# Optimization experiments

Measured on AMD Instinct MI355X. Metric: run time of the kernel, lower is better.

Reference implementation:

```python
import jax, jax.numpy as jnp
import numpy as np

N, R, B, OUT, STD = 512, 4, 65536, 512, 0.01


def setup_inputs() -> dict:
    key = jax.random.key(0)
    ks = jax.random.split(key, 6)
    return {
        "x": jax.random.normal(ks[0], (B, N), jnp.float32),
        "G": jax.random.normal(ks[1], (N, R), jnp.float32) * STD,
        "H": jax.random.normal(ks[2], (N, R), jnp.float32) * STD,
        "b1": jax.random.normal(ks[3], (N,), jnp.float32) * STD,
        "W2": jax.random.normal(ks[4], (N, OUT), jnp.float32) * STD,
        "b2": jax.random.normal(ks[5], (OUT,), jnp.float32) * STD,
    }


def _shift_A(v):
    # Z_1 v: circular shift down with corner +1 (Toeplitz-like operator A)
    return jnp.concatenate([v[-1:], v[:-1]], axis=0)


def _shift_BT(v):
    # Z_{-1}^T v: shift up with corner -1 (Toeplitz-like operator B^T)
    return jnp.concatenate([v[1:], -v[:1]], axis=0)


def _krylov(shift_fn, V):
    # K[j, :, i] = A^j v_i, shape (n, n, r)
    def step(v, _):
        return shift_fn(v), v
    _, K = jax.lax.scan(step, V, None, length=V.shape[0])
    return K


def krylov_recon(G, H):
    # W = sum_i Krylov(Z_1, g_i) @ Krylov(Z_{-1}^T, h_i)^T, shape (n, n)
    KA = _krylov(_shift_A, G)   # (n, n, r)
    KB = _krylov(_shift_BT, H)  # (n, n, r)
    return jnp.einsum('jai,jbi->ab', KA, KB)


def reference(x, G, H, b1, W2, b2):
    W = krylov_recon(G, H)                 # (n, n) structured matrix
    h = jax.nn.relu(x @ W + b1)            # (B, n)
    return h @ W2 + b2                     # (B, out)
```

## Files before the change

### kernel.cpp

```cpp
#include <hip/hip_runtime.h>
#include <hip/hip_bf16.h>
#include <stdint.h>


typedef __attribute__((ext_vector_type(8))) short bf16x8;
typedef __attribute__((ext_vector_type(4))) float f32x4;
typedef __attribute__((ext_vector_type(4))) unsigned int u32x4;

__device__ __forceinline__ unsigned short f2bf(float f) {
  return __builtin_bit_cast(unsigned short, __float2bfloat16(f));
}

__global__ void build_w_partials(const float* __restrict__ G, const float* __restrict__ H,
                                 float* __restrict__ Wp) {
  __shared__ float4 Gs[512];
  __shared__ float4 Hs[512];
  const int t = threadIdx.x;
  const float4* G4 = (const float4*)G;
  const float4* H4 = (const float4*)H;
  for (int i = t; i < 512; i += 256) { Gs[i] = G4[i]; Hs[i] = H4[i]; }
  __syncthreads();

  const int blk  = blockIdx.x;
  const int tile = blk >> 2;
  const int jc   = blk & 3;
  const int a0 = (tile >> 3) << 6;
  const int b0 = (tile & 7) << 6;
  const int ab = a0 + ((t >> 4) << 2);
  const int bb = b0 + ((t & 15) << 2);

  float acc[4][4] = {};
  const int j0 = jc << 7;
  for (int jj = 0; jj < 128; ++jj) {
    const int j = j0 + jj;
    float4 Ga[4], Hb[4];
#pragma unroll
    for (int r = 0; r < 4; ++r) Ga[r] = Gs[(ab + r - j) & 511];
#pragma unroll
    for (int c = 0; c < 4; ++c) {
      const int idx = bb + c + j;
      const float s = (idx >= 512) ? -1.f : 1.f;
      const float4 hv = Hs[idx & 511];
      Hb[c].x = hv.x * s; Hb[c].y = hv.y * s; Hb[c].z = hv.z * s; Hb[c].w = hv.w * s;
    }
#pragma unroll
    for (int r = 0; r < 4; ++r)
#pragma unroll
      for (int c = 0; c < 4; ++c)
        acc[r][c] += Ga[r].x * Hb[c].x + Ga[r].y * Hb[c].y +
                     Ga[r].z * Hb[c].z + Ga[r].w * Hb[c].w;
  }

  float* outp = Wp + (size_t)jc * 262144;
#pragma unroll
  for (int r = 0; r < 4; ++r)
#pragma unroll
    for (int c = 0; c < 4; ++c)
      outp[(size_t)(ab + r) * 512 + (bb + c)] = acc[r][c];
}

__global__ void reduce_transpose_w(const float* __restrict__ Wp, unsigned short* __restrict__ Wt) {
  const int idx = blockIdx.x * 256 + threadIdx.x;
  const int b = idx >> 9, a = idx & 511;
  const size_t o = (size_t)a * 512 + b;
  float s = Wp[o] + Wp[o + 262144] + Wp[o + 524288] + Wp[o + 786432];
  Wt[(size_t)b * 512 + a] = f2bf(s);
}

__global__ void transpose_convert_w2(const float* __restrict__ W2, unsigned short* __restrict__ W2t) {
  const int idx = blockIdx.x * 256 + threadIdx.x;
  const int n = idx >> 9, k = idx & 511;
  W2t[(size_t)n * 512 + k] = f2bf(W2[(size_t)k * 512 + n]);
}

template <bool AF32>
__global__ __launch_bounds__(512, 2) void gemm_pipe(
    const void* __restrict__ Ap, const unsigned short* __restrict__ Bt,
    const float* __restrict__ bias, void* __restrict__ Cp) {
  constexpr int NT    = 16;
  constexpr int ASLOT = AF32 ? 32768 : 16384;
  constexpr int ARING = AF32 ? 3 : 4;
  constexpr int BSLOT = 16384;
  constexpr int BRING = AF32 ? 3 : 4;
  constexpr int DIST  = AF32 ? 2 : 3;
  constexpr int NAG   = AF32 ? 4 : 2;
  constexpr int BBASE = ARING * ASLOT;

  __shared__ __attribute__((aligned(16))) char lds[ARING * ASLOT + BRING * BSLOT];

  const int tid  = threadIdx.x;
  const int lane = tid & 63;
  const int w    = tid >> 6;
  const int wm   = w & 1;
  const int wn   = w >> 1;
  const int lr   = lane & 15;
  const int lq   = lane >> 4;

  const int bid = (int)blockIdx.x;
  const int wg  = (bid & 7) * 64 + (bid >> 3);
  const int m0  = (wg >> 1) << 8;
  const int n0  = (wg & 1) << 8;

  float bv[4];
#pragma unroll
  for (int ni = 0; ni < 4; ++ni) bv[ni] = bias[n0 + wn * 64 + ni * 16 + lr];
  asm volatile("s_waitcnt vmcnt(0)" ::: "memory");

  size_t aSrcOff[NAG];
  if constexpr (AF32) {
#pragma unroll
    for (int i = 0; i < 4; ++i) {
      const int r = i * 64 + (tid >> 3);
      const int s = tid & 7;
      const int c = s ^ (r & 7);
      aSrcOff[i] = (size_t)r * 2048 + (size_t)(c << 4);
    }
  } else {
#pragma unroll
    for (int i = 0; i < 2; ++i) {
      const int r = i * 128 + (tid >> 2);
      const int s = tid & 3;
      const int c = s ^ ((r >> 1) & 3);
      aSrcOff[i] = (size_t)r * 1024 + (size_t)(c << 4);
    }
  }
  size_t bSrcOff[2];
#pragma unroll
  for (int i = 0; i < 2; ++i) {
    const int r = i * 128 + (tid >> 2);
    const int s = tid & 3;
    const int c = s ^ ((r >> 1) & 3);
    bSrcOff[i] = (size_t)r * 1024 + (size_t)(c << 4);
  }
  const char* aBase = (const char*)Ap + (size_t)m0 * (AF32 ? 2048 : 1024);
  const char* bBase = (const char*)Bt + (size_t)n0 * 1024;

  auto stageA = [&](int kt) {
    const int sl = kt % ARING;
#pragma unroll
    for (int i = 0; i < NAG; ++i)
      __builtin_amdgcn_global_load_lds(
        (const __attribute__((address_space(1))) void*)
          (aBase + aSrcOff[i] + (size_t)kt * (AF32 ? 128 : 64)),
        (__attribute__((address_space(3))) void*)(lds + sl * ASLOT + i * 8192 + w * 1024),
        16, 0, 0);
  };
  auto stageB = [&](int kt) {
    const int sl = kt % BRING;
#pragma unroll
    for (int i = 0; i < 2; ++i)
      __builtin_amdgcn_global_load_lds(
        (const __attribute__((address_space(1))) void*)
          (bBase + bSrcOff[i] + (size_t)kt * 64),
        (__attribute__((address_space(3))) void*)(lds + BBASE + sl * BSLOT + i * 8192 + w * 1024),
        16, 0, 0);
  };

  int offA[8], offB[4];
#pragma unroll
  for (int mi = 0; mi < 8; ++mi) {
    const int r = wm * 128 + mi * 16 + lr;
    if constexpr (AF32)
      offA[mi] = r * 128 + (((2 * lq) ^ (r & 7)) << 4);
    else
      offA[mi] = r * 64 + ((lq ^ ((r >> 1) & 3)) << 4);
  }
#pragma unroll
  for (int ni = 0; ni < 4; ++ni) {
    const int rb = wn * 64 + ni * 16 + lr;
    offB[ni] = rb * 64 + ((lq ^ ((rb >> 1) & 3)) << 4);
  }

  f32x4 acc[8][4];
  const f32x4 vz = {0.f, 0.f, 0.f, 0.f};
#pragma unroll
  for (int i = 0; i < 8; ++i)
#pragma unroll
    for (int j = 0; j < 4; ++j) acc[i][j] = vz;

  stageA(0); stageB(0); stageA(1); stageB(1);
  if constexpr (!AF32) { stageA(2); stageB(2); }
  if constexpr (AF32) asm volatile("s_waitcnt vmcnt(6)" ::: "memory");
  else                asm volatile("s_waitcnt vmcnt(8)" ::: "memory");
  __builtin_amdgcn_s_barrier();
  __builtin_amdgcn_sched_barrier(0);

#pragma unroll
  for (int t = 0; t < NT; ++t) {
    const char* aS = lds + (t % ARING) * ASLOT;
    const char* bS = lds + BBASE + (t % BRING) * BSLOT;
    bf16x8 bfr[4];

    {
#pragma unroll
      for (int ni = 0; ni < 4; ++ni) bfr[ni] = *(const bf16x8*)(bS + offB[ni]);
      bf16x8 afr[4];
      f32x4 lo[4], hi[4];
      if constexpr (AF32) {
#pragma unroll
        for (int k = 0; k < 4; ++k) {
          lo[k] = *(const f32x4*)(aS + offA[k]);
          hi[k] = *(const f32x4*)(aS + (offA[k] ^ 16));
        }
      } else {
#pragma unroll
        for (int k = 0; k < 4; ++k) afr[k] = *(const bf16x8*)(aS + offA[k]);
      }
      if (t + DIST < NT) stageA(t + DIST);
      __builtin_amdgcn_s_barrier();
      asm volatile("s_waitcnt lgkmcnt(0)" ::: "memory");
      __builtin_amdgcn_sched_barrier(0);
      if constexpr (AF32) {
#pragma unroll
        for (int k = 0; k < 4; ++k) {
          unsigned int w0, w1, w2, w3;
          asm("v_cvt_pk_bf16_f32 %0, %1, %2" : "=v"(w0) : "v"(lo[k].x), "v"(lo[k].y));
          asm("v_cvt_pk_bf16_f32 %0, %1, %2" : "=v"(w1) : "v"(lo[k].z), "v"(lo[k].w));
          asm("v_cvt_pk_bf16_f32 %0, %1, %2" : "=v"(w2) : "v"(hi[k].x), "v"(hi[k].y));
          asm("v_cvt_pk_bf16_f32 %0, %1, %2" : "=v"(w3) : "v"(hi[k].z), "v"(hi[k].w));
          u32x4 pw = {w0, w1, w2, w3};
          afr[k] = __builtin_bit_cast(bf16x8, pw);
        }
      }
      __builtin_amdgcn_s_setprio(1);
#pragma unroll
      for (int k = 0; k < 4; ++k)
#pragma unroll
        for (int ni = 0; ni < 4; ++ni)
          acc[k][ni] = __builtin_amdgcn_mfma_f32_16x16x32_bf16(afr[k], bfr[ni], acc[k][ni], 0, 0, 0);
      __builtin_amdgcn_s_setprio(0);
      __builtin_amdgcn_s_barrier();
      __builtin_amdgcn_sched_barrier(0);
    }

    {
      bf16x8 afr[4];
      f32x4 lo[4], hi[4];
      if constexpr (AF32) {
#pragma unroll
        for (int k = 0; k < 4; ++k) {
          lo[k] = *(const f32x4*)(aS + offA[4 + k]);
          hi[k] = *(const f32x4*)(aS + (offA[4 + k] ^ 16));
        }
      } else {
#pragma unroll
        for (int k = 0; k < 4; ++k) afr[k] = *(const bf16x8*)(aS + offA[4 + k]);
      }
      if (t + DIST < NT) stageB(t + DIST);
      __builtin_amdgcn_s_barrier();
      asm volatile("s_waitcnt lgkmcnt(0)" ::: "memory");
      __builtin_amdgcn_sched_barrier(0);
      if constexpr (AF32) {
#pragma unroll
        for (int k = 0; k < 4; ++k) {
          unsigned int w0, w1, w2, w3;
          asm("v_cvt_pk_bf16_f32 %0, %1, %2" : "=v"(w0) : "v"(lo[k].x), "v"(lo[k].y));
          asm("v_cvt_pk_bf16_f32 %0, %1, %2" : "=v"(w1) : "v"(lo[k].z), "v"(lo[k].w));
          asm("v_cvt_pk_bf16_f32 %0, %1, %2" : "=v"(w2) : "v"(hi[k].x), "v"(hi[k].y));
          asm("v_cvt_pk_bf16_f32 %0, %1, %2" : "=v"(w3) : "v"(hi[k].z), "v"(hi[k].w));
          u32x4 pw = {w0, w1, w2, w3};
          afr[k] = __builtin_bit_cast(bf16x8, pw);
        }
      }
      __builtin_amdgcn_s_setprio(1);
#pragma unroll
      for (int k = 0; k < 4; ++k)
#pragma unroll
        for (int ni = 0; ni < 4; ++ni)
          acc[4 + k][ni] = __builtin_amdgcn_mfma_f32_16x16x32_bf16(afr[k], bfr[ni], acc[4 + k][ni], 0, 0, 0);
      __builtin_amdgcn_s_setprio(0);
      if constexpr (AF32) {
        if (t <= NT - 3)      asm volatile("s_waitcnt vmcnt(6)" ::: "memory");
        else if (t == NT - 2) asm volatile("s_waitcnt vmcnt(0)" ::: "memory");
      } else {
        if (t <= NT - 4)      asm volatile("s_waitcnt vmcnt(8)" ::: "memory");
        else if (t == NT - 3) asm volatile("s_waitcnt vmcnt(4)" ::: "memory");
        else if (t == NT - 2) asm volatile("s_waitcnt vmcnt(0)" ::: "memory");
      }
      __builtin_amdgcn_s_barrier();
      __builtin_amdgcn_sched_barrier(0);
    }
  }

#pragma unroll
  for (int ni = 0; ni < 4; ++ni) {
    const int gc = n0 + wn * 64 + ni * 16 + lr;
#pragma unroll
    for (int mi = 0; mi < 8; ++mi) {
      const int gr = m0 + wm * 128 + mi * 16 + lq * 4;
      const f32x4 v = acc[mi][ni];
#pragma unroll
      for (int i = 0; i < 4; ++i) {
        const float val = v[i] + bv[ni];
        if constexpr (AF32)
          ((unsigned short*)Cp)[(size_t)(gr + i) * 512 + gc] = f2bf(val > 0.f ? val : 0.f);
        else
          ((float*)Cp)[(size_t)(gr + i) * 512 + gc] = val;
      }
    }
  }
}

extern "C" void kernel_launch(void* const* d_in, const int* in_sizes, int n_in,
                              void* d_out, int out_size, void* d_ws, size_t ws_size,
                              hipStream_t stream) {
  (void)in_sizes; (void)n_in; (void)out_size; (void)ws_size;
  const float* x  = (const float*)d_in[0];
  const float* G  = (const float*)d_in[1];
  const float* H  = (const float*)d_in[2];
  const float* b1 = (const float*)d_in[3];
  const float* W2 = (const float*)d_in[4];
  const float* b2 = (const float*)d_in[5];
  float* out = (float*)d_out;

  char* ws = (char*)d_ws;
  unsigned short* h   = (unsigned short*)ws;
  unsigned short* Wt  = (unsigned short*)(ws + 67108864);
  unsigned short* W2t = (unsigned short*)(ws + 67633152);
  float*          Wp  = (float*)(ws + 68157440);

  build_w_partials<<<256, 256, 0, stream>>>(G, H, Wp);
  reduce_transpose_w<<<1024, 256, 0, stream>>>(Wp, Wt);
  transpose_convert_w2<<<1024, 256, 0, stream>>>(W2, W2t);
  gemm_pipe<true><<<512, 512, 0, stream>>>((const void*)x, Wt, b1, (void*)h);
  gemm_pipe<false><<<512, 512, 0, stream>>>((const void*)h, W2t, b2, (void*)out);
}
```

Before: 168.7 us.

## Merge A/B staging into unified ring slots with one barrier per k-step

Replaces the separate A and B LDS rings and their split half-step staging with a single ring, where each slot holds both A and B tiles. Each k-step now issues one combined prefetch at the top and ends with one computed vmcnt wait and one barrier, instead of four barriers per step. The bf16 second GEMM loads all eight A fragments at once and issues all 32 MFMAs in a single burst. This cuts barrier and synchronisation overhead, but the prefetch now happens at a different point in the step, which may change how well loads overlap with compute and how many registers are live at once.

Result: no change. 172.0 us (+2.0%).

```diff
diff --git a/kernel.cpp b/kernel.cpp
--- a/kernel.cpp
+++ b/kernel.cpp
@@ -74,19 +74,18 @@
 }
 
 template <bool AF32>
-__global__ __launch_bounds__(512, 2) void gemm_pipe(
+__global__ __launch_bounds__(512, 2) void gemm_ring(
     const void* __restrict__ Ap, const unsigned short* __restrict__ Bt,
     const float* __restrict__ bias, void* __restrict__ Cp) {
   constexpr int NT    = 16;
+  constexpr int RING  = AF32 ? 3 : 4;
   constexpr int ASLOT = AF32 ? 32768 : 16384;
-  constexpr int ARING = AF32 ? 3 : 4;
   constexpr int BSLOT = 16384;
-  constexpr int BRING = AF32 ? 3 : 4;
-  constexpr int DIST  = AF32 ? 2 : 3;
+  constexpr int SLOT  = ASLOT + BSLOT;
   constexpr int NAG   = AF32 ? 4 : 2;
-  constexpr int BBASE = ARING * ASLOT;
-
-  __shared__ __attribute__((aligned(16))) char lds[ARING * ASLOT + BRING * BSLOT];
+  constexpr int GPT   = NAG + 2;
+
+  __shared__ __attribute__((aligned(16))) char lds[RING * SLOT];
 
   const int tid  = threadIdx.x;
   const int lane = tid & 63;
@@ -110,49 +109,43 @@
   if constexpr (AF32) {
 #pragma unroll
     for (int i = 0; i < 4; ++i) {
-      const int r = i * 64 + (tid >> 3);
-      const int s = tid & 7;
-      const int c = s ^ (r & 7);
-      aSrcOff[i] = (size_t)r * 2048 + (size_t)(c << 4);
+      const int cl = i * 512 + tid;
+      const int r = cl >> 3, d = cl & 7;
+      aSrcOff[i] = (size_t)r * 2048 + (size_t)((d ^ (r & 7)) << 4);
     }
   } else {
 #pragma unroll
     for (int i = 0; i < 2; ++i) {
-      const int r = i * 128 + (tid >> 2);
-      const int s = tid & 3;
-      const int c = s ^ ((r >> 1) & 3);
-      aSrcOff[i] = (size_t)r * 1024 + (size_t)(c << 4);
+      const int cl = i * 512 + tid;
+      const int r = cl >> 2, d = cl & 3;
+      aSrcOff[i] = (size_t)r * 1024 + (size_t)((d ^ ((r >> 1) & 3)) << 4);
     }
   }
   size_t bSrcOff[2];
 #pragma unroll
   for (int i = 0; i < 2; ++i) {
-    const int r = i * 128 + (tid >> 2);
-    const int s = tid & 3;
-    const int c = s ^ ((r >> 1) & 3);
-    bSrcOff[i] = (size_t)r * 1024 + (size_t)(c << 4);
+    const int cl = i * 512 + tid;
+    const int r = cl >> 2, d = cl & 3;
+    bSrcOff[i] = (size_t)r * 1024 + (size_t)((d ^ ((r >> 1) & 3)) << 4);
   }
   const char* aBase = (const char*)Ap + (size_t)m0 * (AF32 ? 2048 : 1024);
   const char* bBase = (const char*)Bt + (size_t)n0 * 1024;
 
-  auto stageA = [&](int kt) {
-    const int sl = kt % ARING;
+  auto stage = [&](int kt) {
+    char* sb = lds + (kt % RING) * SLOT;
 #pragma unroll
     for (int i = 0; i < NAG; ++i)
       __builtin_amdgcn_global_load_lds(
         (const __attribute__((address_space(1))) void*)
           (aBase + aSrcOff[i] + (size_t)kt * (AF32 ? 128 : 64)),
-        (__attribute__((address_space(3))) void*)(lds + sl * ASLOT + i * 8192 + w * 1024),
+        (__attribute__((address_space(3))) void*)(sb + i * 8192 + w * 1024),
         16, 0, 0);
-  };
-  auto stageB = [&](int kt) {
-    const int sl = kt % BRING;
 #pragma unroll
     for (int i = 0; i < 2; ++i)
       __builtin_amdgcn_global_load_lds(
         (const __attribute__((address_space(1))) void*)
           (bBase + bSrcOff[i] + (size_t)kt * 64),
-        (__attribute__((address_space(3))) void*)(lds + BBASE + sl * BSLOT + i * 8192 + w * 1024),
+        (__attribute__((address_space(3))) void*)(sb + ASLOT + i * 8192 + w * 1024),
         16, 0, 0);
   };
 
@@ -168,7 +161,7 @@
 #pragma unroll
   for (int ni = 0; ni < 4; ++ni) {
     const int rb = wn * 64 + ni * 16 + lr;
-    offB[ni] = rb * 64 + ((lq ^ ((rb >> 1) & 3)) << 4);
+    offB[ni] = ASLOT + rb * 64 + ((lq ^ ((rb >> 1) & 3)) << 4);
   }
 
   f32x4 acc[8][4];
@@ -178,8 +171,8 @@
 #pragma unroll
     for (int j = 0; j < 4; ++j) acc[i][j] = vz;
 
-  stageA(0); stageB(0); stageA(1); stageB(1);
-  if constexpr (!AF32) { stageA(2); stageB(2); }
+#pragma unroll
+  for (int p = 0; p < RING - 1; ++p) stage(p);
   if constexpr (AF32) asm volatile("s_waitcnt vmcnt(6)" ::: "memory");
   else                asm volatile("s_waitcnt vmcnt(8)" ::: "memory");
   __builtin_amdgcn_s_barrier();
@@ -187,40 +180,32 @@
 
 #pragma unroll
   for (int t = 0; t < NT; ++t) {
-    const char* aS = lds + (t % ARING) * ASLOT;
-    const char* bS = lds + BBASE + (t % BRING) * BSLOT;
+    if (t + RING - 1 < NT) stage(t + RING - 1);
+
+    const char* sb = lds + (t % RING) * SLOT;
     bf16x8 bfr[4];
-
-    {
-#pragma unroll
-      for (int ni = 0; ni < 4; ++ni) bfr[ni] = *(const bf16x8*)(bS + offB[ni]);
-      bf16x8 afr[4];
+#pragma unroll
+    for (int ni = 0; ni < 4; ++ni) bfr[ni] = *(const bf16x8*)(sb + offB[ni]);
+
+    if constexpr (AF32) {
       f32x4 lo[4], hi[4];
-      if constexpr (AF32) {
-#pragma unroll
-        for (int k = 0; k < 4; ++k) {
-          lo[k] = *(const f32x4*)(aS + offA[k]);
-          hi[k] = *(const f32x4*)(aS + (offA[k] ^ 16));
-        }
-      } else {
-#pragma unroll
-        for (int k = 0; k < 4; ++k) afr[k] = *(const bf16x8*)(aS + offA[k]);
-      }
-      if (t + DIST < NT) stageA(t + DIST);
-      __builtin_amdgcn_s_barrier();
+#pragma unroll
+      for (int k = 0; k < 4; ++k) {
+        lo[k] = *(const f32x4*)(sb + offA[k]);
+        hi[k] = *(const f32x4*)(sb + (offA[k] ^ 16));
+      }
       asm volatile("s_waitcnt lgkmcnt(0)" ::: "memory");
       __builtin_amdgcn_sched_barrier(0);
-      if constexpr (AF32) {
-#pragma unroll
-        for (int k = 0; k < 4; ++k) {
-          unsigned int w0, w1, w2, w3;
-          asm("v_cvt_pk_bf16_f32 %0, %1, %2" : "=v"(w0) : "v"(lo[k].x), "v"(lo[k].y));
-          asm("v_cvt_pk_bf16_f32 %0, %1, %2" : "=v"(w1) : "v"(lo[k].z), "v"(lo[k].w));
-          asm("v_cvt_pk_bf16_f32 %0, %1, %2" : "=v"(w2) : "v"(hi[k].x), "v"(hi[k].y));
-          asm("v_cvt_pk_bf16_f32 %0, %1, %2" : "=v"(w3) : "v"(hi[k].z), "v"(hi[k].w));
-          u32x4 pw = {w0, w1, w2, w3};
-          afr[k] = __builtin_bit_cast(bf16x8, pw);
-        }
+      bf16x8 afr[4];
+#pragma unroll
+      for (int k = 0; k < 4; ++k) {
+        unsigned int w0, w1, w2, w3;
+        asm("v_cvt_pk_bf16_f32 %0, %1, %2" : "=v"(w0) : "v"(lo[k].x), "v"(lo[k].y));
+        asm("v_cvt_pk_bf16_f32 %0, %1, %2" : "=v"(w1) : "v"(lo[k].z), "v"(lo[k].w));
+        asm("v_cvt_pk_bf16_f32 %0, %1, %2" : "=v"(w2) : "v"(hi[k].x), "v"(hi[k].y));
+        asm("v_cvt_pk_bf16_f32 %0, %1, %2" : "=v"(w3) : "v"(hi[k].z), "v"(hi[k].w));
+        u32x4 pw = {w0, w1, w2, w3};
+        afr[k] = __builtin_bit_cast(bf16x8, pw);
       }
       __builtin_amdgcn_s_setprio(1);
 #pragma unroll
@@ -229,38 +214,22 @@
         for (int ni = 0; ni < 4; ++ni)
           acc[k][ni] = __builtin_amdgcn_mfma_f32_16x16x32_bf16(afr[k], bfr[ni], acc[k][ni], 0, 0, 0);
       __builtin_amdgcn_s_setprio(0);
-      __builtin_amdgcn_s_barrier();
-      __builtin_amdgcn_sched_barrier(0);
-    }
-
-    {
-      bf16x8 afr[4];
-      f32x4 lo[4], hi[4];
-      if constexpr (AF32) {
-#pragma unroll
-        for (int k = 0; k < 4; ++k) {
-          lo[k] = *(const f32x4*)(aS + offA[4 + k]);
-          hi[k] = *(const f32x4*)(aS + (offA[4 + k] ^ 16));
-        }
-      } else {
-#pragma unroll
-        for (int k = 0; k < 4; ++k) afr[k] = *(const bf16x8*)(aS + offA[4 + k]);
-      }
-      if (t + DIST < NT) stageB(t + DIST);
-      __builtin_amdgcn_s_barrier();
+#pragma unroll
+      for (int k = 0; k < 4; ++k) {
+        lo[k] = *(const f32x4*)(sb + offA[4 + k]);
+        hi[k] = *(const f32x4*)(sb + (offA[4 + k] ^ 16));
+      }
       asm volatile("s_waitcnt lgkmcnt(0)" ::: "memory");
       __builtin_amdgcn_sched_barrier(0);
-      if constexpr (AF32) {
-#pragma unroll
-        for (int k = 0; k < 4; ++k) {
-          unsigned int w0, w1, w2, w3;
-          asm("v_cvt_pk_bf16_f32 %0, %1, %2" : "=v"(w0) : "v"(lo[k].x), "v"(lo[k].y));
-          asm("v_cvt_pk_bf16_f32 %0, %1, %2" : "=v"(w1) : "v"(lo[k].z), "v"(lo[k].w));
-          asm("v_cvt_pk_bf16_f32 %0, %1, %2" : "=v"(w2) : "v"(hi[k].x), "v"(hi[k].y));
-          asm("v_cvt_pk_bf16_f32 %0, %1, %2" : "=v"(w3) : "v"(hi[k].z), "v"(hi[k].w));
-          u32x4 pw = {w0, w1, w2, w3};
-          afr[k] = __builtin_bit_cast(bf16x8, pw);
-        }
+#pragma unroll
+      for (int k = 0; k < 4; ++k) {
+        unsigned int w0, w1, w2, w3;
+        asm("v_cvt_pk_bf16_f32 %0, %1, %2" : "=v"(w0) : "v"(lo[k].x), "v"(lo[k].y));
+        asm("v_cvt_pk_bf16_f32 %0, %1, %2" : "=v"(w1) : "v"(lo[k].z), "v"(lo[k].w));
+        asm("v_cvt_pk_bf16_f32 %0, %1, %2" : "=v"(w2) : "v"(hi[k].x), "v"(hi[k].y));
+        asm("v_cvt_pk_bf16_f32 %0, %1, %2" : "=v"(w3) : "v"(hi[k].z), "v"(hi[k].w));
+        u32x4 pw = {w0, w1, w2, w3};
+        afr[k] = __builtin_bit_cast(bf16x8, pw);
       }
       __builtin_amdgcn_s_setprio(1);
 #pragma unroll
@@ -269,17 +238,31 @@
         for (int ni = 0; ni < 4; ++ni)
           acc[4 + k][ni] = __builtin_amdgcn_mfma_f32_16x16x32_bf16(afr[k], bfr[ni], acc[4 + k][ni], 0, 0, 0);
       __builtin_amdgcn_s_setprio(0);
-      if constexpr (AF32) {
-        if (t <= NT - 3)      asm volatile("s_waitcnt vmcnt(6)" ::: "memory");
-        else if (t == NT - 2) asm volatile("s_waitcnt vmcnt(0)" ::: "memory");
-      } else {
-        if (t <= NT - 4)      asm volatile("s_waitcnt vmcnt(8)" ::: "memory");
-        else if (t == NT - 3) asm volatile("s_waitcnt vmcnt(4)" ::: "memory");
-        else if (t == NT - 2) asm volatile("s_waitcnt vmcnt(0)" ::: "memory");
-      }
-      __builtin_amdgcn_s_barrier();
+    } else {
+      bf16x8 afr[8];
+#pragma unroll
+      for (int k = 0; k < 8; ++k) afr[k] = *(const bf16x8*)(sb + offA[k]);
+      asm volatile("s_waitcnt lgkmcnt(0)" ::: "memory");
       __builtin_amdgcn_sched_barrier(0);
-    }
+      __builtin_amdgcn_s_setprio(1);
+#pragma unroll
+      for (int k = 0; k < 8; ++k)
+#pragma unroll
+        for (int ni = 0; ni < 4; ++ni)
+          acc[k][ni] = __builtin_amdgcn_mfma_f32_16x16x32_bf16(afr[k], bfr[ni], acc[k][ni], 0, 0, 0);
+      __builtin_amdgcn_s_setprio(0);
+    }
+
+    if (t < NT - 1) {
+      const int rem  = NT - 2 - t;
+      const int keep = (rem < RING - 2 ? rem : RING - 2) * GPT;
+      if (keep == 8)      asm volatile("s_waitcnt vmcnt(8)" ::: "memory");
+      else if (keep == 6) asm volatile("s_waitcnt vmcnt(6)" ::: "memory");
+      else if (keep == 4) asm volatile("s_waitcnt vmcnt(4)" ::: "memory");
+      else                asm volatile("s_waitcnt vmcnt(0)" ::: "memory");
+    }
+    __builtin_amdgcn_s_barrier();
+    __builtin_amdgcn_sched_barrier(0);
   }
 
 #pragma unroll
@@ -322,6 +305,6 @@
   build_w_partials<<<256, 256, 0, stream>>>(G, H, Wp);
   reduce_transpose_w<<<1024, 256, 0, stream>>>(Wp, Wt);
   transpose_convert_w2<<<1024, 256, 0, stream>>>(W2, W2t);
-  gemm_pipe<true><<<512, 512, 0, stream>>>((const void*)x, Wt, b1, (void*)h);
-  gemm_pipe<false><<<512, 512, 0, stream>>>((const void*)h, W2t, b2, (void*)out);
-}
+  gemm_ring<true><<<512, 512, 0, stream>>>((const void*)x, Wt, b1, (void*)h);
+  gemm_ring<false><<<512, 512, 0, stream>>>((const void*)h, W2t, b2, (void*)out);
+}
```
